# Kernel optimization log

Hardware: AMD Instinct MI355X
Metric: run time of the kernel (lower is better)

Reference implementation:

```python
import jax, jax.numpy as jnp
import numpy as np

N_NODES = 100000
N_EDGES = 1600000
HIDDEN = 64


def gcn_conv(x, edge_index, W, b):
    """PyG GCNConv: add self-loops, symmetric deg^{-1/2} normalization, scatter-add."""
    n = x.shape[0]
    h = x @ W  # [N, F_out]
    loop = jnp.arange(n, dtype=edge_index.dtype)
    src = jnp.concatenate([edge_index[0], loop])  # [E+N]
    dst = jnp.concatenate([edge_index[1], loop])
    deg = jax.ops.segment_sum(jnp.ones_like(dst, dtype=h.dtype), dst, num_segments=n)
    dinv = jnp.where(deg > 0, jax.lax.rsqrt(jnp.maximum(deg, 1e-12)), 0.0)
    norm = dinv[src] * dinv[dst]  # [E+N]
    msg = h[src] * norm[:, None]  # gather + scale
    out = jax.ops.segment_sum(msg, dst, num_segments=n)  # scatter-add
    return out + b


def setup_inputs() -> dict:
    key = jax.random.key(0)
    k = jax.random.split(key, 6)
    x = jax.random.normal(k[0], (N_NODES, HIDDEN), dtype=jnp.float32)
    edge_index = jax.random.randint(k[1], (2, N_EDGES), 0, N_NODES, dtype=jnp.int32)
    s = 1.0 / np.sqrt(HIDDEN)
    W1 = jax.random.normal(k[2], (HIDDEN, HIDDEN), dtype=jnp.float32) * s
    b1 = jnp.zeros((HIDDEN,), dtype=jnp.float32)
    W2 = jax.random.normal(k[3], (HIDDEN, HIDDEN), dtype=jnp.float32) * s
    b2 = jnp.zeros((HIDDEN,), dtype=jnp.float32)
    return {"x": x, "edge_index": edge_index, "W1": W1, "b1": b1, "W2": W2, "b2": b2}


def reference(x, edge_index, W1, b1, W2, b2):
    # Faithful to source: conv1 applied twice, relu, dropout (eval -> identity), conv2, log_softmax.
    h = gcn_conv(x, edge_index, W1, b1)
    h = jax.nn.relu(gcn_conv(h, edge_index, W1, b1))
    # F.dropout(training=self.training): identity in eval mode
    h = gcn_conv(h, edge_index, W2, b2)
    return jax.nn.log_softmax(h, axis=1)
```

## Files before the change

kernel.cpp:

```cpp
#include <hip/hip_runtime.h>
#include <hip/hip_bf16.h>

#define HID 64

typedef float f32x4 __attribute__((ext_vector_type(4)));

__device__ __forceinline__ unsigned short f2bf(float f) {
    unsigned u = __float_as_uint(f);
    return (unsigned short)((u + 0x7fffu + ((u >> 16) & 1u)) >> 16);
}
__device__ __forceinline__ void acc8(float* a, uint4 v) {
    a[0] += __uint_as_float(v.x << 16);
    a[1] += __uint_as_float(v.x & 0xffff0000u);
    a[2] += __uint_as_float(v.y << 16);
    a[3] += __uint_as_float(v.y & 0xffff0000u);
    a[4] += __uint_as_float(v.z << 16);
    a[5] += __uint_as_float(v.z & 0xffff0000u);
    a[6] += __uint_as_float(v.w << 16);
    a[7] += __uint_as_float(v.w & 0xffff0000u);
}


__global__ __launch_bounds__(256) void hist_part_kernel(
    const int* __restrict__ dst, int* __restrict__ cnt, int E, int psz) {
    int part = blockIdx.x & 7, chunk = blockIdx.x >> 3;
    int i = chunk * 256 + threadIdx.x;
    if (i >= E) return;
    int d = __builtin_nontemporal_load(&dst[i]);
    if (d / psz == part) atomicAdd(&cnt[d], 1);
}

__global__ __launch_bounds__(256) void bsum_kernel(const int* __restrict__ cnt,
                                                   int* __restrict__ bsums, int N) {
    __shared__ int s[256];
    int tid = threadIdx.x, i = blockIdx.x * 256 + tid;
    s[tid] = (i < N) ? cnt[i] : 0;
    __syncthreads();
    for (int o = 128; o > 0; o >>= 1) {
        if (tid < o) s[tid] += s[tid + o];
        __syncthreads();
    }
    if (tid == 0) bsums[blockIdx.x] = s[0];
}

__global__ __launch_bounds__(512) void scan_bsums_kernel(int* __restrict__ bsums, int nblk) {
    __shared__ int s[512];
    int tid = threadIdx.x;
    int orig = (tid < nblk) ? bsums[tid] : 0;
    s[tid] = orig;
    __syncthreads();
    for (int off = 1; off < 512; off <<= 1) {
        int v = (tid >= off) ? s[tid - off] : 0;
        __syncthreads();
        s[tid] += v;
        __syncthreads();
    }
    if (tid < nblk) bsums[tid] = s[tid] - orig;
}

__global__ __launch_bounds__(256) void rowptr_kernel(
    const int* __restrict__ cnt, const int* __restrict__ bsums,
    int4* __restrict__ nodeinfo, int* __restrict__ cursor, int N) {
    __shared__ int s[256];
    int tid = threadIdx.x, i = blockIdx.x * 256 + tid;
    int c = (i < N) ? cnt[i] : 0;
    s[tid] = c;
    __syncthreads();
    for (int off = 1; off < 256; off <<= 1) {
        int v = (tid >= off) ? s[tid - off] : 0;
        __syncthreads();
        s[tid] += v;
        __syncthreads();
    }
    if (i < N) {
        int excl = s[tid] - c + bsums[blockIdx.x];
        cursor[i] = excl;
        int4 ni;
        ni.x = excl;
        ni.y = c;
        ni.z = (int)__float_as_uint(rsqrtf((float)c + 1.0f));
        ni.w = 0;
        nodeinfo[i] = ni;
    }
}

__global__ __launch_bounds__(256) void fill_part_kernel(
    const int* __restrict__ src, const int* __restrict__ dst,
    int* __restrict__ cursor, int* __restrict__ col, int E, int psz) {
    int part = blockIdx.x & 7, chunk = blockIdx.x >> 3;
    int i = chunk * 256 + threadIdx.x;
    if (i >= E) return;
    int d = __builtin_nontemporal_load(&dst[i]);
    if (d / psz == part) {
        int s = __builtin_nontemporal_load(&src[i]);
        int p = atomicAdd(&cursor[d], 1);
        col[p] = s;
    }
}

__device__ __forceinline__ void gather64_pre(
    const uint4* __restrict__ g4, const int* __restrict__ col,
    int beg, int deg, int c, int n, int N, int lane, float* t) {
    int eighth = lane >> 3, fo = lane & 7;
    float a0[8] = {}, a1[8] = {};
    int base = 0;
    while (true) {
        int rem = deg - base; if (rem > 64) rem = 64;
        int groups = (rem + 7) >> 3;
        int j = 0;
        for (; j + 2 <= groups; j += 2) {
            int s0 = __shfl(c, 8 * (j + 0) + eighth, 64);
            int s1 = __shfl(c, 8 * (j + 1) + eighth, 64);
            uint4 v0 = g4[(size_t)s0 * 8 + fo];
            uint4 v1 = g4[(size_t)s1 * 8 + fo];
            acc8(a0, v0); acc8(a1, v1);
        }
        if (j < groups) {
            int s0 = __shfl(c, 8 * j + eighth, 64);
            uint4 v0 = g4[(size_t)s0 * 8 + fo];
            acc8(a0, v0);
        }
        base += 64;
        if (base >= deg) break;
        int r2 = deg - base;
        c = (lane < r2) ? __builtin_nontemporal_load(&col[beg + base + lane]) : N;
    }
    float sf[8] = {};
    acc8(sf, g4[(size_t)n * 8 + fo]);
#pragma unroll
    for (int k = 0; k < 8; ++k) {
        float s = a0[k] + a1[k];
        s += __shfl_xor(s, 8, 64);
        s += __shfl_xor(s, 16, 64);
        s += __shfl_xor(s, 32, 64);
        t[k] = s + sf[k];
    }
}


__global__ __launch_bounds__(256) void gemm_scale_kernel(
    const float* __restrict__ X, const float* __restrict__ W,
    const int4* __restrict__ nodeinfo, unsigned short* __restrict__ g, int N) {
    __shared__ float Ws[HID * HID];
    __shared__ float xs[4][HID];
    int tid = threadIdx.x;
    for (int i = tid; i < HID * HID; i += 256) Ws[i] = W[i];
    __syncthreads();
    int w = tid >> 6, c = tid & 63;
    float* xsw = xs[w];
    int ngrp = (N + 3) / 4;
    for (int grp = blockIdx.x; grp < ngrp; grp += gridDim.x) {
        int row = grp * 4 + w;
        if (row >= N) continue;
        xsw[c] = __builtin_nontemporal_load(&X[(size_t)row * HID + c]);
        float dn = __uint_as_float((unsigned)__builtin_amdgcn_readfirstlane(nodeinfo[row].z));
        float acc = 0.f;
#pragma unroll
        for (int k = 0; k < HID; ++k) acc = fmaf(xsw[k], Ws[k * HID + c], acc);
        __builtin_nontemporal_store(f2bf(acc * dn), &g[(size_t)row * HID + c]);
    }
}


template <bool RELU>
__global__ __launch_bounds__(256, 4) void agg_gemm_kernel(
    const unsigned short* __restrict__ g_in, const int4* __restrict__ nodeinfo,
    const int* __restrict__ col, const float* __restrict__ bias,
    const float* __restrict__ W, unsigned short* __restrict__ g_out, int N) {
    int tid = threadIdx.x, w = tid >> 6, lane = tid & 63;
    int s = lane & 7, q = lane >> 3;
    unsigned Wp[32];
#pragma unroll
    for (int j = 0; j < 8; ++j)
#pragma unroll
        for (int i2 = 0; i2 < 4; ++i2) {
            float w0 = W[(8 * s + j) * HID + 8 * q + 2 * i2];
            float w1 = W[(8 * s + j) * HID + 8 * q + 2 * i2 + 1];
            Wp[j * 4 + i2] = (unsigned)f2bf(w0) | ((unsigned)f2bf(w1) << 16);
        }
    float bb[8];
#pragma unroll
    for (int j = 0; j < 8; ++j) bb[j] = bias[8 * s + j];
    const uint4* g4 = (const uint4*)g_in;
    const int ngrp = (N + 3) / 4;
    for (int grp = blockIdx.x; grp < ngrp; grp += gridDim.x) {
        int n = grp * 4 + w;
        if (n >= N) continue;
        int4 ni = nodeinfo[n];
        int beg = __builtin_amdgcn_readfirstlane(ni.x);
        int deg = __builtin_amdgcn_readfirstlane(ni.y);
        float dn = __uint_as_float((unsigned)__builtin_amdgcn_readfirstlane(ni.z));
        int c0 = (lane < deg) ? __builtin_nontemporal_load(&col[beg + lane]) : N;
        float t[8];
        gather64_pre(g4, col, beg, deg, c0, n, N, lane, t);
        float o[8];
#pragma unroll
        for (int j = 0; j < 8; ++j) {
            o[j] = fmaf(dn, t[j], bb[j]);
            if (RELU) o[j] = fmaxf(o[j], 0.f);
        }
        float p[8] = {};
#pragma unroll
        for (int j = 0; j < 8; ++j) {
            float oj = o[j];
#pragma unroll
            for (int i2 = 0; i2 < 4; ++i2) {
                unsigned wv = Wp[j * 4 + i2];
                p[2 * i2]     = fmaf(oj, __uint_as_float(wv << 16), p[2 * i2]);
                p[2 * i2 + 1] = fmaf(oj, __uint_as_float(wv & 0xffff0000u), p[2 * i2 + 1]);
            }
        }
        bool b0 = (s & 1) != 0;
        float q1[4];
#pragma unroll
        for (int m = 0; m < 4; ++m) {
            float A = __shfl_xor(p[2 * m], 1, 64);
            float B = __shfl_xor(p[2 * m + 1], 1, 64);
            q1[m] = b0 ? (p[2 * m + 1] + B) : (p[2 * m] + A);
        }
        bool b1 = ((s >> 1) & 1) != 0;
        float q2[2];
#pragma unroll
        for (int m = 0; m < 2; ++m) {
            float A = __shfl_xor(q1[2 * m], 2, 64);
            float B = __shfl_xor(q1[2 * m + 1], 2, 64);
            q2[m] = b1 ? (q1[2 * m + 1] + B) : (q1[2 * m] + A);
        }
        bool b2 = ((s >> 2) & 1) != 0;
        float A = __shfl_xor(q2[0], 4, 64);
        float B = __shfl_xor(q2[1], 4, 64);
        float res = b2 ? (q2[1] + B) : (q2[0] + A);
        __builtin_nontemporal_store(f2bf(res * dn), &g_out[(size_t)n * HID + lane]);
    }
}


__global__ __launch_bounds__(256) void agg_lsm_kernel(
    const unsigned short* __restrict__ g_in, const int4* __restrict__ nodeinfo,
    const int* __restrict__ col, const float* __restrict__ bias,
    float* __restrict__ out, int N) {
    int tid = threadIdx.x, w = tid >> 6, lane = tid & 63;
    int eighth = lane >> 3, fo = lane & 7;
    const uint4* g4 = (const uint4*)g_in;
    float bb[8];
#pragma unroll
    for (int j = 0; j < 8; ++j) bb[j] = bias[8 * fo + j];
    const int ngrp = (N + 3) / 4;
    for (int grp = blockIdx.x; grp < ngrp; grp += gridDim.x) {
        int n = grp * 4 + w;
        if (n >= N) continue;
        int4 ni = nodeinfo[n];
        int beg = __builtin_amdgcn_readfirstlane(ni.x);
        int deg = __builtin_amdgcn_readfirstlane(ni.y);
        float dn = __uint_as_float((unsigned)__builtin_amdgcn_readfirstlane(ni.z));
        int c0 = (lane < deg) ? __builtin_nontemporal_load(&col[beg + lane]) : N;
        float t[8];
        gather64_pre(g4, col, beg, deg, c0, n, N, lane, t);
        float v[8];
#pragma unroll
        for (int k = 0; k < 8; ++k) v[k] = fmaf(dn, t[k], bb[k]);
        float mx = v[0];
#pragma unroll
        for (int k = 1; k < 8; ++k) mx = fmaxf(mx, v[k]);
        mx = fmaxf(mx, __shfl_xor(mx, 1, 64));
        mx = fmaxf(mx, __shfl_xor(mx, 2, 64));
        mx = fmaxf(mx, __shfl_xor(mx, 4, 64));
        float sum = 0.f;
#pragma unroll
        for (int k = 0; k < 8; ++k) sum += expf(v[k] - mx);
        sum += __shfl_xor(sum, 1, 64);
        sum += __shfl_xor(sum, 2, 64);
        sum += __shfl_xor(sum, 4, 64);
        float ls = mx + logf(sum);
        if (eighth == 0) {
            f32x4 o0 = {v[0] - ls, v[1] - ls, v[2] - ls, v[3] - ls};
            f32x4 o1 = {v[4] - ls, v[5] - ls, v[6] - ls, v[7] - ls};
            f32x4* op = (f32x4*)out;
            __builtin_nontemporal_store(o0, &op[(size_t)n * 16 + 2 * fo]);
            __builtin_nontemporal_store(o1, &op[(size_t)n * 16 + 2 * fo + 1]);
        }
    }
}


static inline size_t alignup(size_t x) { return (x + 255) & ~(size_t)255; }

extern "C" void kernel_launch(void* const* d_in, const int* in_sizes, int n_in,
                              void* d_out, int out_size, void* d_ws, size_t ws_size,
                              hipStream_t stream) {
    const float* x  = (const float*)d_in[0];
    const int*   ei = (const int*)d_in[1];
    const float* W1 = (const float*)d_in[2];
    const float* b1 = (const float*)d_in[3];
    const float* W2 = (const float*)d_in[4];
    const float* b2 = (const float*)d_in[5];

    const int N = in_sizes[0] / HID;
    const int E = in_sizes[1] / 2;
    const int* src = ei;
    const int* dst = ei + E;

    const int nblk = (N + 255) / 256;
    const int psz  = (N + 7) / 8;

    char* w = (char*)d_ws;
    unsigned short* gA       = (unsigned short*)w; w += alignup((size_t)(N + 1) * HID * 2);
    unsigned short* gB       = (unsigned short*)w; w += alignup((size_t)(N + 1) * HID * 2);
    int4*           nodeinfo = (int4*)w;           w += alignup((size_t)N * 16);
    int*            cnt      = (int*)w;            w += alignup((size_t)N * 4);
    int*            cursor   = (int*)w;            w += alignup((size_t)N * 4);
    int*            col      = (int*)w;            w += alignup((size_t)E * 4);
    int*            bsums    = (int*)w;            w += alignup((size_t)nblk * 4);

    const int egrid  = (E + 255) / 256;
    const int gsgrid = 2048;

    (void)hipMemsetAsync(gA + (size_t)N * HID, 0, HID * sizeof(unsigned short), stream);
    (void)hipMemsetAsync(gB + (size_t)N * HID, 0, HID * sizeof(unsigned short), stream);

    (void)hipMemsetAsync(cnt, 0, (size_t)N * sizeof(int), stream);
    hist_part_kernel<<<egrid * 8, 256, 0, stream>>>(dst, cnt, E, psz);
    bsum_kernel<<<nblk, 256, 0, stream>>>(cnt, bsums, N);
    scan_bsums_kernel<<<1, 512, 0, stream>>>(bsums, nblk);
    rowptr_kernel<<<nblk, 256, 0, stream>>>(cnt, bsums, nodeinfo, cursor, N);
    fill_part_kernel<<<egrid * 8, 256, 0, stream>>>(src, dst, cursor, col, E, psz);

    gemm_scale_kernel<<<gsgrid, 256, 0, stream>>>(x, W1, nodeinfo, gA, N);
    agg_gemm_kernel<false><<<gsgrid, 256, 0, stream>>>(gA, nodeinfo, col, b1, W1, gB, N);
    agg_gemm_kernel<true><<<gsgrid, 256, 0, stream>>>(gB, nodeinfo, col, b1, W2, gA, N);
    agg_lsm_kernel<<<gsgrid, 256, 0, stream>>>(gA, nodeinfo, col, b2, (float*)d_out, N);
}
```

Measured before the change: 415.4 us.

## Switch aggregation gather to one-feature-per-lane with scalar column loads

```diff
diff --git a/kernel.cpp b/kernel.cpp
--- a/kernel.cpp
+++ b/kernel.cpp
@@ -9,15 +9,8 @@
     unsigned u = __float_as_uint(f);
     return (unsigned short)((u + 0x7fffu + ((u >> 16) & 1u)) >> 16);
 }
-__device__ __forceinline__ void acc8(float* a, uint4 v) {
-    a[0] += __uint_as_float(v.x << 16);
-    a[1] += __uint_as_float(v.x & 0xffff0000u);
-    a[2] += __uint_as_float(v.y << 16);
-    a[3] += __uint_as_float(v.y & 0xffff0000u);
-    a[4] += __uint_as_float(v.z << 16);
-    a[5] += __uint_as_float(v.z & 0xffff0000u);
-    a[6] += __uint_as_float(v.w << 16);
-    a[7] += __uint_as_float(v.w & 0xffff0000u);
+__device__ __forceinline__ float bfu(unsigned short u) {
+    return __uint_as_float(((unsigned)u) << 16);
 }
 
 
@@ -98,45 +91,6 @@
     }
 }
 
-__device__ __forceinline__ void gather64_pre(
-    const uint4* __restrict__ g4, const int* __restrict__ col,
-    int beg, int deg, int c, int n, int N, int lane, float* t) {
-    int eighth = lane >> 3, fo = lane & 7;
-    float a0[8] = {}, a1[8] = {};
-    int base = 0;
-    while (true) {
-        int rem = deg - base; if (rem > 64) rem = 64;
-        int groups = (rem + 7) >> 3;
-        int j = 0;
-        for (; j + 2 <= groups; j += 2) {
-            int s0 = __shfl(c, 8 * (j + 0) + eighth, 64);
-            int s1 = __shfl(c, 8 * (j + 1) + eighth, 64);
-            uint4 v0 = g4[(size_t)s0 * 8 + fo];
-            uint4 v1 = g4[(size_t)s1 * 8 + fo];
-            acc8(a0, v0); acc8(a1, v1);
-        }
-        if (j < groups) {
-            int s0 = __shfl(c, 8 * j + eighth, 64);
-            uint4 v0 = g4[(size_t)s0 * 8 + fo];
-            acc8(a0, v0);
-        }
-        base += 64;
-        if (base >= deg) break;
-        int r2 = deg - base;
-        c = (lane < r2) ? __builtin_nontemporal_load(&col[beg + base + lane]) : N;
-    }
-    float sf[8] = {};
-    acc8(sf, g4[(size_t)n * 8 + fo]);
-#pragma unroll
-    for (int k = 0; k < 8; ++k) {
-        float s = a0[k] + a1[k];
-        s += __shfl_xor(s, 8, 64);
-        s += __shfl_xor(s, 16, 64);
-        s += __shfl_xor(s, 32, 64);
-        t[k] = s + sf[k];
-    }
-}
-
 
 __global__ __launch_bounds__(256) void gemm_scale_kernel(
     const float* __restrict__ X, const float* __restrict__ W,
@@ -161,9 +115,69 @@
     }
 }
 
+__device__ __forceinline__ float gather_lane(
+    const unsigned short* __restrict__ gb, const int* __restrict__ col,
+    int beg, int deg, int n, int lane) {
+    float a0 = 0.f, a1 = 0.f, a2 = 0.f, a3 = 0.f;
+    int j = 0;
+#pragma unroll 2
+    for (; j + 4 <= deg; j += 4) {
+        int s0 = col[beg + j + 0];
+        int s1 = col[beg + j + 1];
+        int s2 = col[beg + j + 2];
+        int s3 = col[beg + j + 3];
+        unsigned short u0 = gb[(size_t)s0 * HID + lane];
+        unsigned short u1 = gb[(size_t)s1 * HID + lane];
+        unsigned short u2 = gb[(size_t)s2 * HID + lane];
+        unsigned short u3 = gb[(size_t)s3 * HID + lane];
+        a0 += bfu(u0); a1 += bfu(u1); a2 += bfu(u2); a3 += bfu(u3);
+    }
+    for (; j < deg; ++j) {
+        int s0 = col[beg + j];
+        a0 += bfu(gb[(size_t)s0 * HID + lane]);
+    }
+    a0 += bfu(gb[(size_t)n * HID + lane]);
+    return (a0 + a1) + (a2 + a3);
+}
+
+__device__ __forceinline__ float reggemm_butterfly(
+    const unsigned* Wp, const float* o, int s) {
+    float p[8] = {};
+#pragma unroll
+    for (int j = 0; j < 8; ++j) {
+        float oj = o[j];
+#pragma unroll
+        for (int i2 = 0; i2 < 4; ++i2) {
+            unsigned wv = Wp[j * 4 + i2];
+            p[2 * i2]     = fmaf(oj, __uint_as_float(wv << 16), p[2 * i2]);
+            p[2 * i2 + 1] = fmaf(oj, __uint_as_float(wv & 0xffff0000u), p[2 * i2 + 1]);
+        }
+    }
+    bool b0 = (s & 1) != 0;
+    float q1[4];
+#pragma unroll
+    for (int m = 0; m < 4; ++m) {
+        float A = __shfl_xor(p[2 * m], 1, 64);
+        float B = __shfl_xor(p[2 * m + 1], 1, 64);
+        q1[m] = b0 ? (p[2 * m + 1] + B) : (p[2 * m] + A);
+    }
+    bool b1 = ((s >> 1) & 1) != 0;
+    float q2[2];
+#pragma unroll
+    for (int m = 0; m < 2; ++m) {
+        float A = __shfl_xor(q1[2 * m], 2, 64);
+        float B = __shfl_xor(q1[2 * m + 1], 2, 64);
+        q2[m] = b1 ? (q1[2 * m + 1] + B) : (q1[2 * m] + A);
+    }
+    bool b2 = ((s >> 2) & 1) != 0;
+    float A = __shfl_xor(q2[0], 4, 64);
+    float B = __shfl_xor(q2[1], 4, 64);
+    return b2 ? (q2[1] + B) : (q2[0] + A);
+}
+
 
 template <bool RELU>
-__global__ __launch_bounds__(256, 4) void agg_gemm_kernel(
+__global__ __launch_bounds__(256, 2) void agg_gemm_kernel(
     const unsigned short* __restrict__ g_in, const int4* __restrict__ nodeinfo,
     const int* __restrict__ col, const float* __restrict__ bias,
     const float* __restrict__ W, unsigned short* __restrict__ g_out, int N) {
@@ -181,7 +195,6 @@
     float bb[8];
 #pragma unroll
     for (int j = 0; j < 8; ++j) bb[j] = bias[8 * s + j];
-    const uint4* g4 = (const uint4*)g_in;
     const int ngrp = (N + 3) / 4;
     for (int grp = blockIdx.x; grp < ngrp; grp += gridDim.x) {
         int n = grp * 4 + w;
@@ -190,47 +203,18 @@
         int beg = __builtin_amdgcn_readfirstlane(ni.x);
         int deg = __builtin_amdgcn_readfirstlane(ni.y);
         float dn = __uint_as_float((unsigned)__builtin_amdgcn_readfirstlane(ni.z));
-        int c0 = (lane < deg) ? __builtin_nontemporal_load(&col[beg + lane]) : N;
+        float acc = gather_lane(g_in, col, beg, deg, n, lane);
         float t[8];
-        gather64_pre(g4, col, beg, deg, c0, n, N, lane, t);
+#pragma unroll
+        for (int j = 0; j < 8; ++j) t[j] = __shfl(acc, 8 * s + j, 64);
         float o[8];
 #pragma unroll
         for (int j = 0; j < 8; ++j) {
             o[j] = fmaf(dn, t[j], bb[j]);
             if (RELU) o[j] = fmaxf(o[j], 0.f);
         }
-        float p[8] = {};
-#pragma unroll
-        for (int j = 0; j < 8; ++j) {
-            float oj = o[j];
-#pragma unroll
-            for (int i2 = 0; i2 < 4; ++i2) {
-                unsigned wv = Wp[j * 4 + i2];
-                p[2 * i2]     = fmaf(oj, __uint_as_float(wv << 16), p[2 * i2]);
-                p[2 * i2 + 1] = fmaf(oj, __uint_as_float(wv & 0xffff0000u), p[2 * i2 + 1]);
-            }
-        }
-        bool b0 = (s & 1) != 0;
-        float q1[4];
-#pragma unroll
-        for (int m = 0; m < 4; ++m) {
-            float A = __shfl_xor(p[2 * m], 1, 64);
-            float B = __shfl_xor(p[2 * m + 1], 1, 64);
-            q1[m] = b0 ? (p[2 * m + 1] + B) : (p[2 * m] + A);
-        }
-        bool b1 = ((s >> 1) & 1) != 0;
-        float q2[2];
-#pragma unroll
-        for (int m = 0; m < 2; ++m) {
-            float A = __shfl_xor(q1[2 * m], 2, 64);
-            float B = __shfl_xor(q1[2 * m + 1], 2, 64);
-            q2[m] = b1 ? (q1[2 * m + 1] + B) : (q1[2 * m] + A);
-        }
-        bool b2 = ((s >> 2) & 1) != 0;
-        float A = __shfl_xor(q2[0], 4, 64);
-        float B = __shfl_xor(q2[1], 4, 64);
-        float res = b2 ? (q2[1] + B) : (q2[0] + A);
-        __builtin_nontemporal_store(f2bf(res * dn), &g_out[(size_t)n * HID + lane]);
+        float r = reggemm_butterfly(Wp, o, s);
+        __builtin_nontemporal_store(f2bf(r * dn), &g_out[(size_t)n * HID + lane]);
     }
 }
 
@@ -240,11 +224,7 @@
     const int* __restrict__ col, const float* __restrict__ bias,
     float* __restrict__ out, int N) {
     int tid = threadIdx.x, w = tid >> 6, lane = tid & 63;
-    int eighth = lane >> 3, fo = lane & 7;
-    const uint4* g4 = (const uint4*)g_in;
-    float bb[8];
-#pragma unroll
-    for (int j = 0; j < 8; ++j) bb[j] = bias[8 * fo + j];
+    float bl = bias[lane];
     const int ngrp = (N + 3) / 4;
     for (int grp = blockIdx.x; grp < ngrp; grp += gridDim.x) {
         int n = grp * 4 + w;
@@ -253,32 +233,15 @@
         int beg = __builtin_amdgcn_readfirstlane(ni.x);
         int deg = __builtin_amdgcn_readfirstlane(ni.y);
         float dn = __uint_as_float((unsigned)__builtin_amdgcn_readfirstlane(ni.z));
-        int c0 = (lane < deg) ? __builtin_nontemporal_load(&col[beg + lane]) : N;
-        float t[8];
-        gather64_pre(g4, col, beg, deg, c0, n, N, lane, t);
-        float v[8];
-#pragma unroll
-        for (int k = 0; k < 8; ++k) v[k] = fmaf(dn, t[k], bb[k]);
-        float mx = v[0];
-#pragma unroll
-        for (int k = 1; k < 8; ++k) mx = fmaxf(mx, v[k]);
-        mx = fmaxf(mx, __shfl_xor(mx, 1, 64));
-        mx = fmaxf(mx, __shfl_xor(mx, 2, 64));
-        mx = fmaxf(mx, __shfl_xor(mx, 4, 64));
-        float sum = 0.f;
-#pragma unroll
-        for (int k = 0; k < 8; ++k) sum += expf(v[k] - mx);
-        sum += __shfl_xor(sum, 1, 64);
-        sum += __shfl_xor(sum, 2, 64);
-        sum += __shfl_xor(sum, 4, 64);
-        float ls = mx + logf(sum);
-        if (eighth == 0) {
-            f32x4 o0 = {v[0] - ls, v[1] - ls, v[2] - ls, v[3] - ls};
-            f32x4 o1 = {v[4] - ls, v[5] - ls, v[6] - ls, v[7] - ls};
-            f32x4* op = (f32x4*)out;
-            __builtin_nontemporal_store(o0, &op[(size_t)n * 16 + 2 * fo]);
-            __builtin_nontemporal_store(o1, &op[(size_t)n * 16 + 2 * fo + 1]);
-        }
+        float t = gather_lane(g_in, col, beg, deg, n, lane);
+        float v = fmaf(dn, t, bl);
+        float mx = v;
+#pragma unroll
+        for (int o = 1; o < 64; o <<= 1) mx = fmaxf(mx, __shfl_xor(mx, o, 64));
+        float sum = expf(v - mx);
+#pragma unroll
+        for (int o = 1; o < 64; o <<= 1) sum += __shfl_xor(sum, o, 64);
+        __builtin_nontemporal_store(v - mx - logf(sum), &out[(size_t)n * HID + lane]);
     }
 }
 
@@ -315,9 +278,6 @@
     const int egrid  = (E + 255) / 256;
     const int gsgrid = 2048;
 
-    (void)hipMemsetAsync(gA + (size_t)N * HID, 0, HID * sizeof(unsigned short), stream);
-    (void)hipMemsetAsync(gB + (size_t)N * HID, 0, HID * sizeof(unsigned short), stream);
-
     (void)hipMemsetAsync(cnt, 0, (size_t)N * sizeof(int), stream);
     hist_part_kernel<<<egrid * 8, 256, 0, stream>>>(dst, cnt, E, psz);
     bsum_kernel<<<nblk, 256, 0, stream>>>(cnt, bsums, N);
```

Result: no change. 419.9 us (+1.1%).
